# Optimization experiments

Measured on AMD Instinct MI355X. Metric: run time of the kernel, lower is better.

Reference implementation:

```python
import jax, jax.numpy as jnp
import numpy as np

N = 512          # hidden size n
B = 256          # batch
T = 512          # timesteps
INPUT_SIZE = 2
RANK = 2
ALPHA = 0.2
SIGMA_IN = 0.2
SIGMA_REC = 0.15


def setup_inputs() -> dict:
    key = jax.random.key(0)
    k1, k2, k3, k4, k5, k6 = jax.random.split(key, 6)
    u = jax.random.normal(k1, (B, T, INPUT_SIZE), dtype=jnp.float32)
    # standard normal; scaled by sqrt(2/alpha*sigma_in^2) inside reference
    input_noise = jax.random.normal(k2, (B, T, INPUT_SIZE), dtype=jnp.float32)
    # in the repo this is sigma_rec * randn projected on PCs; plain scaled randn here
    recurrent_noise = SIGMA_REC * jax.random.normal(k3, (B, T, N), dtype=jnp.float32)
    # low-rank recurrent weight: W_rec = A @ B, entries ~ U(-0.1, 0.1)
    A = 0.1 * (2.0 * jax.random.uniform(k4, (N, RANK), dtype=jnp.float32) - 1.0)
    Bm = 0.1 * (2.0 * jax.random.uniform(k5, (RANK, N), dtype=jnp.float32) - 1.0)
    W_rec = A @ Bm
    b_rec = jnp.zeros((N,), dtype=jnp.float32)  # normal_(std=0) -> zeros
    # nn.Linear default init: U(-1/sqrt(in), 1/sqrt(in))
    bound = 1.0 / np.sqrt(INPUT_SIZE)
    W_in = jax.random.uniform(k6, (N, INPUT_SIZE), dtype=jnp.float32,
                              minval=-bound, maxval=bound)
    return {"u": u, "input_noise": input_noise, "recurrent_noise": recurrent_noise,
            "W_in": W_in, "W_rec": W_rec, "b_rec": b_rec}


def reference(u, input_noise, recurrent_noise, W_in, W_rec, b_rec):
    alpha = ALPHA
    in_scale = np.sqrt(2.0 / ALPHA * SIGMA_IN ** 2).astype(np.float32)
    # inputs = input_layer(u + input_noise)  -> [B, T, N]
    inputs = jnp.einsum('bti,ni->btn', u + in_scale * input_noise, W_in)
    # scan over first T-1 timesteps, time-major
    xs = (jnp.swapaxes(inputs, 0, 1)[:-1],          # [T-1, B, N]
          jnp.swapaxes(recurrent_noise, 0, 1)[:-1])  # [T-1, B, N]
    s0 = jnp.zeros((u.shape[0], W_rec.shape[0]), dtype=u.dtype)

    def step(s, x):
        inp_t, noise_t = x
        s_new = (1.0 - alpha) * s + alpha * (
            jax.nn.relu(s) @ W_rec.T + b_rec + inp_t + noise_t)
        return s_new, s_new

    _, ys = jax.lax.scan(step, s0, xs)              # [T-1, B, N]
    states = jnp.concatenate([s0[None], ys], axis=0)  # [T, B, N]
    return jnp.swapaxes(states, 0, 1)               # [B, T, N]
```

## Files before the change

### kernel.cpp

```cpp
#include <hip/hip_runtime.h>
#include <math.h>

#define NH 512
#define BATCH 256
#define TT 512
#define NSTEPS 511
#define ALPHA 0.2f
#define OMA 0.8f
#define ISCALE 0.6324555320336759f
#define PD 12

typedef float vf4 __attribute__((ext_vector_type(4)));


__device__ __forceinline__ float wave_reduce_sum(float v) {
#pragma unroll
    for (int m = 32; m >= 1; m >>= 1) v += __shfl_xor(v, m, 64);
    return v;
}

__device__ __forceinline__ unsigned long long enc_key(float v, int i) {
    return (((unsigned long long)__float_as_uint(v)) << 32) | (unsigned int)i;
}

__device__ __forceinline__ unsigned long long wave_max_key(unsigned long long k) {
#pragma unroll
    for (int m = 32; m >= 1; m >>= 1) {
        unsigned long long o = __shfl_xor(k, m, 64);
        k = (o > k) ? o : k;
    }
    return k;
}

__device__ __forceinline__ int scan_argmax_rn(const float* __restrict__ rn, int tid) {
    const float4* rn4 = (const float4*)rn;
    unsigned long long key = 0;
#pragma unroll
    for (int r = 0; r < 2; ++r) {
        float4 v = rn4[tid + 64 * r];
        int base = 4 * (tid + 64 * r);
        unsigned long long k0 = enc_key(v.x, base);
        unsigned long long k1 = enc_key(v.y, base + 1);
        unsigned long long k2 = enc_key(v.z, base + 2);
        unsigned long long k3 = enc_key(v.w, base + 3);
        k0 = k0 > k1 ? k0 : k1;
        k2 = k2 > k3 ? k2 : k3;
        k0 = k0 > k2 ? k0 : k2;
        key = key > k0 ? key : k0;
    }
    return (int)(wave_max_key(key) & 0xffffffffULL);
}

__device__ __forceinline__ float dpp_sum63(float v) {
    v += __int_as_float(__builtin_amdgcn_update_dpp(0, __float_as_int(v), 0x111, 0xf, 0xf, true));
    v += __int_as_float(__builtin_amdgcn_update_dpp(0, __float_as_int(v), 0x112, 0xf, 0xf, true));
    v += __int_as_float(__builtin_amdgcn_update_dpp(0, __float_as_int(v), 0x114, 0xf, 0xf, true));
    v += __int_as_float(__builtin_amdgcn_update_dpp(0, __float_as_int(v), 0x118, 0xf, 0xf, true));
    v += __int_as_float(__builtin_amdgcn_update_dpp(0, __float_as_int(v), 0x142, 0xa, 0xf, true));
    v += __int_as_float(__builtin_amdgcn_update_dpp(0, __float_as_int(v), 0x143, 0xc, 0xf, true));
    return v;
}


__global__ void k_rownorm(const float* __restrict__ W, float* __restrict__ rn) {
    const int i = blockIdx.x, tid = threadIdx.x;
    const float4* row = (const float4*)(W + (size_t)i * NH);
    float acc = 0.f;
#pragma unroll
    for (int r = 0; r < 2; ++r) {
        float4 v = row[tid + 64 * r];
        acc = fmaf(v.x, v.x, fmaf(v.y, v.y, fmaf(v.z, v.z, fmaf(v.w, v.w, acc))));
    }
    acc = wave_reduce_sum(acc);
    if (tid == 0) rn[i] = acc;
}

__global__ void k_rowdot(const float* __restrict__ W, const float* __restrict__ rn,
                         float* __restrict__ dv) {
    const int i = blockIdx.x, tid = threadIdx.x;
    const int i1 = scan_argmax_rn(rn, tid);
    const float4* rowi = (const float4*)(W + (size_t)i * NH);
    const float4* row1 = (const float4*)(W + (size_t)i1 * NH);
    float acc = 0.f;
#pragma unroll
    for (int r = 0; r < 2; ++r) {
        float4 a = rowi[tid + 64 * r];
        float4 b = row1[tid + 64 * r];
        acc = fmaf(a.x, b.x, fmaf(a.y, b.y, fmaf(a.z, b.z, fmaf(a.w, b.w, acc))));
    }
    acc = wave_reduce_sum(acc);
    if (tid == 0) dv[i] = acc;
}

__global__ void k_computeP(const float* __restrict__ W, const float* __restrict__ rn,
                           const float* __restrict__ dv, float* __restrict__ P,
                           int* __restrict__ idx) {
    const int n = blockIdx.x, tid = threadIdx.x;
    const int i1 = scan_argmax_rn(rn, tid);
    const float rn1 = rn[i1];
    const float inv1 = 1.f / rn1;

    const float4* rn4 = (const float4*)rn;
    const float4* dv4 = (const float4*)dv;
    unsigned long long key = 0;
#pragma unroll
    for (int r = 0; r < 2; ++r) {
        float4 a = rn4[tid + 64 * r];
        float4 d = dv4[tid + 64 * r];
        int base = 4 * (tid + 64 * r);
        float r0 = fmaxf(a.x - d.x * d.x * inv1, 0.f);
        float r1 = fmaxf(a.y - d.y * d.y * inv1, 0.f);
        float r2 = fmaxf(a.z - d.z * d.z * inv1, 0.f);
        float r3 = fmaxf(a.w - d.w * d.w * inv1, 0.f);
        unsigned long long k0 = (base + 0 != i1) ? enc_key(r0, base + 0) : 0ULL;
        unsigned long long k1 = (base + 1 != i1) ? enc_key(r1, base + 1) : 0ULL;
        unsigned long long k2 = (base + 2 != i1) ? enc_key(r2, base + 2) : 0ULL;
        unsigned long long k3 = (base + 3 != i1) ? enc_key(r3, base + 3) : 0ULL;
        k0 = k0 > k1 ? k0 : k1;
        k2 = k2 > k3 ? k2 : k3;
        k0 = k0 > k2 ? k0 : k2;
        key = key > k0 ? key : k0;
    }
    const int i2 = (int)(wave_max_key(key) & 0xffffffffULL);

    const float4* rown = (const float4*)(W + (size_t)n * NH);
    const float4* row1 = (const float4*)(W + (size_t)i1 * NH);
    const float4* row2 = (const float4*)(W + (size_t)i2 * NH);
    float t0 = 0.f, t1 = 0.f;
#pragma unroll
    for (int r = 0; r < 2; ++r) {
        float4 a = rown[tid + 64 * r];
        float4 b = row1[tid + 64 * r];
        float4 c = row2[tid + 64 * r];
        t0 = fmaf(a.x, b.x, fmaf(a.y, b.y, fmaf(a.z, b.z, fmaf(a.w, b.w, t0))));
        t1 = fmaf(a.x, c.x, fmaf(a.y, c.y, fmaf(a.z, c.z, fmaf(a.w, c.w, t1))));
    }
    t0 = wave_reduce_sum(t0);
    t1 = wave_reduce_sum(t1);
    if (tid == 0) {
        float g11 = rn1, g22 = rn[i2], g12 = dv[i2];
        float det = fmaf(g11, g22, -g12 * g12);
        float inv = 1.f / det;
        P[2 * n]     = ALPHA * ((g22 * t0 - g12 * t1) * inv);
        P[2 * n + 1] = ALPHA * ((g11 * t1 - g12 * t0) * inv);
        if (n == 0) { idx[0] = i1; idx[1] = i2; }
    }
}

__launch_bounds__(64, 1)
__global__ void k_main(const float* __restrict__ u, const float* __restrict__ inoise,
                       const float* __restrict__ rnoise, const float* __restrict__ W_in,
                       const float* __restrict__ W, const float* __restrict__ b_rec,
                       const int* __restrict__ idx, const float* __restrict__ P,
                       float* __restrict__ out) {
    __shared__ float2 lds_x[TT];
    const int b = blockIdx.x, lane = threadIdx.x;
    const int i1 = idx[0];
    const int i2 = idx[1];

    const float4* u4 = (const float4*)(u + (size_t)b * TT * 2);
    const float4* n4 = (const float4*)(inoise + (size_t)b * TT * 2);
    float4* lx4 = (float4*)lds_x;
#pragma unroll
    for (int r = 0; r < 4; ++r) {
        float4 a = u4[lane + 64 * r];
        float4 c = n4[lane + 64 * r];
        float4 x;
        x.x = fmaf(ISCALE, c.x, a.x);
        x.y = fmaf(ISCALE, c.y, a.y);
        x.z = fmaf(ISCALE, c.z, a.z);
        x.w = fmaf(ISCALE, c.w, a.w);
        lx4[lane + 64 * r] = x;
    }
    __syncthreads();

    const int n0 = lane * 8;
    float aa0[8], aa1[8], q0[8], q1[8], w0[8], w1[8], cb[8], s[8];
#pragma unroll
    for (int j = 0; j < 8; ++j) {
        const int n = n0 + j;
        aa0[j] = P[2 * n];
        aa1[j] = P[2 * n + 1];
        q0[j] = W[(size_t)i1 * NH + n];
        q1[j] = W[(size_t)i2 * NH + n];
        w0[j] = ALPHA * W_in[2 * n];
        w1[j] = ALPHA * W_in[2 * n + 1];
        cb[j] = ALPHA * b_rec[n];
        s[j] = 0.f;
    }

    const float* nzb = rnoise + (size_t)b * TT * NH + n0;
    float* ob = out + (size_t)b * TT * NH + n0;

    vf4 z = {0.f, 0.f, 0.f, 0.f};
    __builtin_nontemporal_store(z, (vf4*)ob);
    __builtin_nontemporal_store(z, (vf4*)(ob + 4));

    float4 bA[PD], bB[PD];
#pragma unroll
    for (int k = 0; k < PD; ++k) {
        bA[k] = *(const float4*)(nzb + (size_t)k * NH);
        bB[k] = *(const float4*)(nzb + (size_t)k * NH + 4);
    }

#define STEP(t_, k_, REFILL_)                                                        \
    {                                                                                \
        const int t = (t_);                                                          \
        float2 x = lds_x[t];                                                         \
        float nz[8];                                                                 \
        nz[0] = bA[k_].x; nz[1] = bA[k_].y; nz[2] = bA[k_].z; nz[3] = bA[k_].w;      \
        nz[4] = bB[k_].x; nz[5] = bB[k_].y; nz[6] = bB[k_].z; nz[7] = bB[k_].w;      \
        if (REFILL_) {                                                               \
            int tp = t + PD; if (tp > NSTEPS) tp = NSTEPS;     \
            bA[k_] = *(const float4*)(nzb + (size_t)tp * NH);                        \
            bB[k_] = *(const float4*)(nzb + (size_t)tp * NH + 4);                    \
        }                                                                            \
        float base_[8], m0[8], m1[8];                                                \
        _Pragma("unroll")                                                            \
        for (int j = 0; j < 8; ++j) {                                                \
            float rs = fmaxf(s[j], 0.f);                                             \
            m0[j] = rs * q0[j];                                                      \
            m1[j] = rs * q1[j];                                                      \
            float v = fmaf(ALPHA, nz[j], cb[j]);                                     \
            v = fmaf(w0[j], x.x, v);                                                 \
            v = fmaf(w1[j], x.y, v);                                                 \
            base_[j] = fmaf(OMA, s[j], v);                                           \
        }                                                                            \
        float a0 = ((m0[0] + m0[1]) + (m0[2] + m0[3])) +                             \
                   ((m0[4] + m0[5]) + (m0[6] + m0[7]));                              \
        float a1 = ((m1[0] + m1[1]) + (m1[2] + m1[3])) +                             \
                   ((m1[4] + m1[5]) + (m1[6] + m1[7]));                              \
        float r0 = dpp_sum63(a0);                                                    \
        float r1 = dpp_sum63(a1);                                                    \
        float p0 = __int_as_float(__builtin_amdgcn_readlane(__float_as_int(r0), 63));\
        float p1 = __int_as_float(__builtin_amdgcn_readlane(__float_as_int(r1), 63));\
        _Pragma("unroll")                                                            \
        for (int j = 0; j < 8; ++j) {                                                \
            float v = fmaf(aa0[j], p0, base_[j]);                                    \
            s[j] = fmaf(aa1[j], p1, v);                                              \
        }                                                                            \
        vf4 oA = {s[0], s[1], s[2], s[3]};                                           \
        vf4 oB = {s[4], s[5], s[6], s[7]};                                           \
        __builtin_nontemporal_store(oA, (vf4*)(ob + (size_t)(t + 1) * NH));          \
        __builtin_nontemporal_store(oB, (vf4*)(ob + (size_t)(t + 1) * NH + 4));      \
    }

    for (int tb = 0; tb < 504; tb += PD) {
#pragma unroll
        for (int k = 0; k < PD; ++k) STEP(tb + k, k, true)
    }
#pragma unroll
    for (int k = 0; k < 7; ++k) STEP(504 + k, k, false)

#undef STEP
}


extern "C" void kernel_launch(void* const* d_in, const int* in_sizes, int n_in,
                              void* d_out, int out_size, void* d_ws, size_t ws_size,
                              hipStream_t stream) {
    const float* u      = (const float*)d_in[0];
    const float* inoise = (const float*)d_in[1];
    const float* rnoise = (const float*)d_in[2];
    const float* W_in   = (const float*)d_in[3];
    const float* W      = (const float*)d_in[4];
    const float* b_rec  = (const float*)d_in[5];
    float* out = (float*)d_out;

    char* ws = (char*)d_ws;
    int* idx  = (int*)(ws + 0);
    float* rn = (float*)(ws + 64);
    float* dv = (float*)(ws + 2112);
    float* P  = (float*)(ws + 4160);

    hipLaunchKernelGGL(k_rownorm, dim3(NH), dim3(64), 0, stream, W, rn);
    hipLaunchKernelGGL(k_rowdot, dim3(NH), dim3(64), 0, stream, W, rn, dv);
    hipLaunchKernelGGL(k_computeP, dim3(NH), dim3(64), 0, stream, W, rn, dv, P, idx);
    hipLaunchKernelGGL(k_main, dim3(BATCH), dim3(64), 0, stream,
                       u, inoise, rnoise, W_in, W, b_rec, idx, P, out);
}
```

Before: 471.1 us.

## Split each batch row across four waves with LDS cross-wave reduction per step

The main recurrence kernel now gives each batch element four wavefronts of 64 lanes, each lane owning 2 hidden units instead of 8. Per-step rank-2 projections are reduced within each wave by DPP, exchanged through double-buffered LDS, and combined after a block barrier. The goal is to shorten each step's serial dependency chain and get more parallel memory traffic for the noise loads and output stores. The cost is a __syncthreads on every one of the 511 timesteps, which may dominate the latency-bound loop. Input values are also now read from LDS in vector batches per block of steps.

```diff
diff --git a/kernel.cpp b/kernel.cpp
--- a/kernel.cpp
+++ b/kernel.cpp
@@ -9,7 +9,9 @@
 #define OMA 0.8f
 #define ISCALE 0.6324555320336759f
 #define PD 12
-
+#define WPB 4
+
+typedef float vf2 __attribute__((ext_vector_type(2)));
 typedef float vf4 __attribute__((ext_vector_type(4)));
 
 
@@ -147,110 +149,116 @@
     }
 }
 
-__launch_bounds__(64, 1)
+__launch_bounds__(256, 1)
 __global__ void k_main(const float* __restrict__ u, const float* __restrict__ inoise,
                        const float* __restrict__ rnoise, const float* __restrict__ W_in,
                        const float* __restrict__ W, const float* __restrict__ b_rec,
                        const int* __restrict__ idx, const float* __restrict__ P,
                        float* __restrict__ out) {
-    __shared__ float2 lds_x[TT];
-    const int b = blockIdx.x, lane = threadIdx.x;
+    __shared__ __align__(16) float2 lds_x[TT];
+    __shared__ __align__(16) float2 lds_p[2][WPB];
+    const int b = blockIdx.x;
+    const int tid = threadIdx.x;
+    const int wid = tid >> 6;
+    const int lane = tid & 63;
     const int i1 = idx[0];
     const int i2 = idx[1];
 
-    const float4* u4 = (const float4*)(u + (size_t)b * TT * 2);
-    const float4* n4 = (const float4*)(inoise + (size_t)b * TT * 2);
-    float4* lx4 = (float4*)lds_x;
-#pragma unroll
-    for (int r = 0; r < 4; ++r) {
-        float4 a = u4[lane + 64 * r];
-        float4 c = n4[lane + 64 * r];
+    {
+        const float4* u4 = (const float4*)(u + (size_t)b * TT * 2);
+        const float4* n4 = (const float4*)(inoise + (size_t)b * TT * 2);
+        float4 a = u4[tid];
+        float4 c = n4[tid];
         float4 x;
         x.x = fmaf(ISCALE, c.x, a.x);
         x.y = fmaf(ISCALE, c.y, a.y);
         x.z = fmaf(ISCALE, c.z, a.z);
         x.w = fmaf(ISCALE, c.w, a.w);
-        lx4[lane + 64 * r] = x;
+        ((float4*)lds_x)[tid] = x;
     }
     __syncthreads();
 
-    const int n0 = lane * 8;
-    float aa0[8], aa1[8], q0[8], q1[8], w0[8], w1[8], cb[8], s[8];
-#pragma unroll
-    for (int j = 0; j < 8; ++j) {
-        const int n = n0 + j;
-        aa0[j] = P[2 * n];
-        aa1[j] = P[2 * n + 1];
-        q0[j] = W[(size_t)i1 * NH + n];
-        q1[j] = W[(size_t)i2 * NH + n];
-        w0[j] = ALPHA * W_in[2 * n];
-        w1[j] = ALPHA * W_in[2 * n + 1];
-        cb[j] = ALPHA * b_rec[n];
-        s[j] = 0.f;
-    }
+    const int n0 = (wid << 7) + (lane << 1);
+    const float q0x = W[(size_t)i1 * NH + n0],     q0y = W[(size_t)i1 * NH + n0 + 1];
+    const float q1x = W[(size_t)i2 * NH + n0],     q1y = W[(size_t)i2 * NH + n0 + 1];
+    const float A0x = P[2 * n0],                   A1x = P[2 * n0 + 1];
+    const float A0y = P[2 * n0 + 2],               A1y = P[2 * n0 + 3];
+    const float w0x = ALPHA * W_in[2 * n0],        w1x = ALPHA * W_in[2 * n0 + 1];
+    const float w0y = ALPHA * W_in[2 * n0 + 2],    w1y = ALPHA * W_in[2 * n0 + 3];
+    const float cbx = ALPHA * b_rec[n0],           cby = ALPHA * b_rec[n0 + 1];
+    float sx = 0.f, sy = 0.f;
 
     const float* nzb = rnoise + (size_t)b * TT * NH + n0;
     float* ob = out + (size_t)b * TT * NH + n0;
 
-    vf4 z = {0.f, 0.f, 0.f, 0.f};
-    __builtin_nontemporal_store(z, (vf4*)ob);
-    __builtin_nontemporal_store(z, (vf4*)(ob + 4));
-
-    float4 bA[PD], bB[PD];
-#pragma unroll
-    for (int k = 0; k < PD; ++k) {
-        bA[k] = *(const float4*)(nzb + (size_t)k * NH);
-        bB[k] = *(const float4*)(nzb + (size_t)k * NH + 4);
-    }
-
-#define STEP(t_, k_, REFILL_)                                                        \
+    vf2 z = {0.f, 0.f};
+    __builtin_nontemporal_store(z, (vf2*)ob);
+
+    vf2 buf[PD];
+#pragma unroll
+    for (int k = 0; k < PD; ++k) buf[k] = *(const vf2*)(nzb + (size_t)k * NH);
+
+#define STEP(t_, k_, REFILL_, XX_, XY_)                                              \
     {                                                                                \
         const int t = (t_);                                                          \
-        float2 x = lds_x[t];                                                         \
-        float nz[8];                                                                 \
-        nz[0] = bA[k_].x; nz[1] = bA[k_].y; nz[2] = bA[k_].z; nz[3] = bA[k_].w;      \
-        nz[4] = bB[k_].x; nz[5] = bB[k_].y; nz[6] = bB[k_].z; nz[7] = bB[k_].w;      \
+        vf2 nz = buf[k_];                                                            \
         if (REFILL_) {                                                               \
             int tp = t + PD; if (tp > NSTEPS) tp = NSTEPS;     \
-            bA[k_] = *(const float4*)(nzb + (size_t)tp * NH);                        \
-            bB[k_] = *(const float4*)(nzb + (size_t)tp * NH + 4);                    \
+            buf[k_] = *(const vf2*)(nzb + (size_t)tp * NH);                          \
         }                                                                            \
-        float base_[8], m0[8], m1[8];                                                \
-        _Pragma("unroll")                                                            \
-        for (int j = 0; j < 8; ++j) {                                                \
-            float rs = fmaxf(s[j], 0.f);                                             \
-            m0[j] = rs * q0[j];                                                      \
-            m1[j] = rs * q1[j];                                                      \
-            float v = fmaf(ALPHA, nz[j], cb[j]);                                     \
-            v = fmaf(w0[j], x.x, v);                                                 \
-            v = fmaf(w1[j], x.y, v);                                                 \
-            base_[j] = fmaf(OMA, s[j], v);                                           \
-        }                                                                            \
-        float a0 = ((m0[0] + m0[1]) + (m0[2] + m0[3])) +                             \
-                   ((m0[4] + m0[5]) + (m0[6] + m0[7]));                              \
-        float a1 = ((m1[0] + m1[1]) + (m1[2] + m1[3])) +                             \
-                   ((m1[4] + m1[5]) + (m1[6] + m1[7]));                              \
-        float r0 = dpp_sum63(a0);                                                    \
-        float r1 = dpp_sum63(a1);                                                    \
-        float p0 = __int_as_float(__builtin_amdgcn_readlane(__float_as_int(r0), 63));\
-        float p1 = __int_as_float(__builtin_amdgcn_readlane(__float_as_int(r1), 63));\
-        _Pragma("unroll")                                                            \
-        for (int j = 0; j < 8; ++j) {                                                \
-            float v = fmaf(aa0[j], p0, base_[j]);                                    \
-            s[j] = fmaf(aa1[j], p1, v);                                              \
-        }                                                                            \
-        vf4 oA = {s[0], s[1], s[2], s[3]};                                           \
-        vf4 oB = {s[4], s[5], s[6], s[7]};                                           \
-        __builtin_nontemporal_store(oA, (vf4*)(ob + (size_t)(t + 1) * NH));          \
-        __builtin_nontemporal_store(oB, (vf4*)(ob + (size_t)(t + 1) * NH + 4));      \
+        const float xx = (XX_);                                                      \
+        const float xy = (XY_);                                                      \
+        float rsx = fmaxf(sx, 0.f), rsy = fmaxf(sy, 0.f);                            \
+        float pa = fmaf(rsy, q0y, rsx * q0x);                                        \
+        float pb = fmaf(rsy, q1y, rsx * q1x);                                        \
+        pa = dpp_sum63(pa);                                                          \
+        pb = dpp_sum63(pb);                                                          \
+             \
+        float bx = fmaf(ALPHA, nz.x, cbx);                                           \
+        bx = fmaf(w0x, xx, bx);                                                      \
+        bx = fmaf(w1x, xy, bx);                                                      \
+        bx = fmaf(OMA, sx, bx);                                                      \
+        float by = fmaf(ALPHA, nz.y, cby);                                           \
+        by = fmaf(w0y, xx, by);                                                      \
+        by = fmaf(w1y, xy, by);                                                      \
+        by = fmaf(OMA, sy, by);                                                      \
+        if (lane == 63) lds_p[(t) & 1][wid] = make_float2(pa, pb);                   \
+        __syncthreads();                                                             \
+        const float4* pp = (const float4*)lds_p[(t) & 1];                            \
+        float4 r0 = pp[0];                                                           \
+        float4 r1 = pp[1];                                                           \
+        float p0 = (r0.x + r0.z) + (r1.x + r1.z);                                    \
+        float p1 = (r0.y + r0.w) + (r1.y + r1.w);                                    \
+        sx = fmaf(A1x, p1, fmaf(A0x, p0, bx));                                       \
+        sy = fmaf(A1y, p1, fmaf(A0y, p0, by));                                       \
+        vf2 o = {sx, sy};                                                            \
+        __builtin_nontemporal_store(o, (vf2*)(ob + (size_t)(t + 1) * NH));           \
     }
 
     for (int tb = 0; tb < 504; tb += PD) {
-#pragma unroll
-        for (int k = 0; k < PD; ++k) STEP(tb + k, k, true)
-    }
-#pragma unroll
-    for (int k = 0; k < 7; ++k) STEP(504 + k, k, false)
+        const float4* lxs = (const float4*)(lds_x + tb);
+        float4 xb[6];
+#pragma unroll
+        for (int r = 0; r < 6; ++r) xb[r] = lxs[r];
+#pragma unroll
+        for (int k = 0; k < PD; ++k) {
+            STEP(tb + k, k, true,
+                 ((k & 1) ? xb[k >> 1].z : xb[k >> 1].x),
+                 ((k & 1) ? xb[k >> 1].w : xb[k >> 1].y))
+        }
+    }
+    {
+        const float4* lxs = (const float4*)(lds_x + 504);
+        float4 xb[4];
+#pragma unroll
+        for (int r = 0; r < 4; ++r) xb[r] = lxs[r];
+#pragma unroll
+        for (int k = 0; k < 7; ++k) {
+            STEP(504 + k, k, false,
+                 ((k & 1) ? xb[k >> 1].z : xb[k >> 1].x),
+                 ((k & 1) ? xb[k >> 1].w : xb[k >> 1].y))
+        }
+    }
 
 #undef STEP
 }
@@ -276,6 +284,6 @@
     hipLaunchKernelGGL(k_rownorm, dim3(NH), dim3(64), 0, stream, W, rn);
     hipLaunchKernelGGL(k_rowdot, dim3(NH), dim3(64), 0, stream, W, rn, dv);
     hipLaunchKernelGGL(k_computeP, dim3(NH), dim3(64), 0, stream, W, rn, dv, P, idx);
-    hipLaunchKernelGGL(k_main, dim3(BATCH), dim3(64), 0, stream,
+    hipLaunchKernelGGL(k_main, dim3(BATCH), dim3(256), 0, stream,
                        u, inoise, rnoise, W_in, W, b_rec, idx, P, out);
 }
```

Result: no change. 470.5 us (-0.1%).
